# Optimization experiments

Hardware: AMD Instinct MI355X
Metric: run time of the kernel (lower is better)

The kernel has to match this reference:

```python
import jax, jax.numpy as jnp
import numpy as np

B, S, D = 4, 4096, 1024
E, H, TOPK = 8, 2752, 2


def setup_inputs() -> dict:
    key = jax.random.key(0)
    k0, k1, k2, k3, k4 = jax.random.split(key, 5)
    x = jax.random.normal(k0, (B, S, D), dtype=jnp.float32)
    gate_w = jax.random.normal(k1, (E, D), dtype=jnp.float32) * 0.02
    w1 = jax.random.normal(k2, (E, H, D), dtype=jnp.float32) * 0.02
    w2 = jax.random.normal(k3, (E, D, H), dtype=jnp.float32) * 0.02
    w3 = jax.random.normal(k4, (E, H, D), dtype=jnp.float32) * 0.02
    return {"x": x, "gate_w": gate_w, "w1": w1, "w2": w2, "w3": w3}


def reference(x, gate_w, w1, w2, w3):
    """MoE layer: softmax router -> top-k (normalized) -> per-expert SwiGLU FFN -> weighted combine."""
    b, s, d = x.shape
    xt = x.reshape(-1, d)                       # [T, D], T = B*S
    logits = xt @ gate_w.T                      # [T, E]
    scores = jax.nn.softmax(logits, axis=-1)
    topk_w, topk_i = jax.lax.top_k(scores, TOPK)  # [T, K]
    topk_w = topk_w / (jnp.sum(topk_w, axis=-1, keepdims=True) + 1e-20)

    y = jnp.zeros_like(xt)
    n_experts = gate_w.shape[0]
    for e in range(n_experts):
        # combine weight for expert e per token (0 if not routed to e)
        we = jnp.sum(jnp.where(topk_i == e, topk_w, 0.0), axis=-1)  # [T]
        h = jax.nn.silu(xt @ w1[e].T) * (xt @ w3[e].T)              # [T, H]
        y = y + we[:, None] * (h @ w2[e].T)                         # [T, D]
    return y.reshape(b, s, d)
```

## Files before the change

### kernel.cpp

```cpp
#include <hip/hip_runtime.h>
#include <hip/hip_bf16.h>
#include <stdint.h>

#define T_TOK 16384
#define D_DIM 1024
#define E_NUM 8
#define H_DIM 2752
#define NSLOT (T_TOK * 2)

typedef __bf16 bf16x8_t __attribute__((ext_vector_type(8)));
typedef float f32x4_t __attribute__((ext_vector_type(4)));

__device__ __forceinline__ uint16_t f2bf(float f) {
    union { float f; uint32_t u; } v; v.f = f;
    return (uint16_t)((v.u + 0x7FFFu + ((v.u >> 16) & 1u)) >> 16);
}
__device__ __forceinline__ ushort4 f4_to_bf4(float4 v) {
    ushort4 r; r.x = f2bf(v.x); r.y = f2bf(v.y); r.z = f2bf(v.z); r.w = f2bf(v.w);
    return r;
}
__device__ __forceinline__ void gl_lds16(const uint16_t* g, uint16_t* l) {
    __builtin_amdgcn_global_load_lds((const __attribute__((address_space(1))) void*)g,
                                     (__attribute__((address_space(3))) void*)l,
                                     16, 0, 0);
}

__global__ __launch_bounds__(256) void router_kernel(
    const float* __restrict__ x, const float* __restrict__ gw,
    int* __restrict__ topk_i, float* __restrict__ topk_w) {
    int tid = threadIdx.x;
    int t = blockIdx.x * 4 + (tid >> 6);
    int lane = tid & 63;
    const float* xr = x + (size_t)t * D_DIM;
    double acc[E_NUM];
#pragma unroll
    for (int e = 0; e < E_NUM; ++e) acc[e] = 0.0;
    for (int k = lane; k < D_DIM; k += 64) {
        double xv = (double)xr[k];
#pragma unroll
        for (int e = 0; e < E_NUM; ++e) acc[e] += xv * (double)gw[e * D_DIM + k];
    }
#pragma unroll
    for (int e = 0; e < E_NUM; ++e) {
        double v = acc[e];
        for (int off = 32; off > 0; off >>= 1) v += __shfl_down(v, off, 64);
        acc[e] = v;
    }
    if (lane == 0) {
        int i0 = 0; double m0 = acc[0];
#pragma unroll
        for (int e = 1; e < E_NUM; ++e) if (acc[e] > m0) { m0 = acc[e]; i0 = e; }
        int i1 = -1; double m1 = -1.0e300;
#pragma unroll
        for (int e = 0; e < E_NUM; ++e) if (e != i0 && acc[e] > m1) { m1 = acc[e]; i1 = e; }
        double e1 = exp(m1 - m0);
        double s = 1.0 + e1;
        topk_i[t * 2 + 0] = i0; topk_i[t * 2 + 1] = i1;
        topk_w[t * 2 + 0] = (float)(1.0 / s);
        topk_w[t * 2 + 1] = (float)(e1 / s);
    }
}

__global__ __launch_bounds__(256) void count_kernel(
    const int* __restrict__ topk_i,
    int* __restrict__ counts_f, int* __restrict__ counts_s) {
    __shared__ int hf[E_NUM], hs[E_NUM];
    int tid = threadIdx.x;
    if (tid < E_NUM) { hf[tid] = 0; hs[tid] = 0; }
    __syncthreads();
    int t = blockIdx.x * 256 + tid;
    atomicAdd(&hf[topk_i[t * 2 + 0]], 1);
    atomicAdd(&hs[topk_i[t * 2 + 1]], 1);
    __syncthreads();
    if (tid < E_NUM) {
        if (hf[tid]) atomicAdd(&counts_f[tid], hf[tid]);
    } else if (tid < 2 * E_NUM) {
        int e = tid - E_NUM;
        if (hs[e]) atomicAdd(&counts_s[e], hs[e]);
    }
}

__global__ void prefix_kernel(const int* __restrict__ cf, const int* __restrict__ cs,
                              int* __restrict__ bases, int* __restrict__ splits,
                              int* __restrict__ cnts) {
    int s = 0;
    for (int e = 0; e < E_NUM; ++e) {
        bases[e] = s;
        splits[e] = s + cf[e];
        cnts[e] = cf[e] + cs[e];
        s += cnts[e];
    }
}

__global__ __launch_bounds__(256) void assign_kernel(
    const int* __restrict__ topk_i, const float* __restrict__ topk_w,
    const int* __restrict__ bases, const int* __restrict__ splits,
    int* __restrict__ fills_f, int* __restrict__ fills_s,
    int* __restrict__ slot_tok, float* __restrict__ slot_w) {
    __shared__ int hf[E_NUM], hs[E_NUM], bf[E_NUM], bs[E_NUM];
    int tid = threadIdx.x;
    if (tid < E_NUM) { hf[tid] = 0; hs[tid] = 0; }
    __syncthreads();
    int t = blockIdx.x * 256 + tid;
    int e0 = topk_i[t * 2 + 0], e1 = topk_i[t * 2 + 1];
    int r0 = atomicAdd(&hf[e0], 1);
    int r1 = atomicAdd(&hs[e1], 1);
    __syncthreads();
    if (tid < E_NUM) {
        bf[tid] = hf[tid] ? atomicAdd(&fills_f[tid], hf[tid]) : 0;
    } else if (tid < 2 * E_NUM) {
        int e = tid - E_NUM;
        bs[e] = hs[e] ? atomicAdd(&fills_s[e], hs[e]) : 0;
    }
    __syncthreads();
    int s0 = bases[e0] + bf[e0] + r0;
    int s1 = splits[e1] + bs[e1] + r1;
    slot_tok[s0] = t; slot_w[s0] = topk_w[t * 2 + 0];
    slot_tok[s1] = t; slot_w[s1] = topk_w[t * 2 + 1];
}

__global__ __launch_bounds__(256) void cvtx_kernel(const float* __restrict__ x,
                                                   uint16_t* __restrict__ Xb) {
    size_t i = (size_t)blockIdx.x * 256 + threadIdx.x;
    ((ushort4*)Xb)[i] = f4_to_bf4(((const float4*)x)[i]);
}
__global__ __launch_bounds__(256) void cvt13_kernel(const float* __restrict__ w1,
                                                    const float* __restrict__ w3,
                                                    uint16_t* __restrict__ w1be,
                                                    uint16_t* __restrict__ w3be, int e) {
    size_t i = (size_t)blockIdx.x * 256 + threadIdx.x;
    const float4* s1 = (const float4*)(w1 + (size_t)e * H_DIM * D_DIM);
    const float4* s3 = (const float4*)(w3 + (size_t)e * H_DIM * D_DIM);
    ((ushort4*)w1be)[i] = f4_to_bf4(s1[i]);
    ((ushort4*)w3be)[i] = f4_to_bf4(s3[i]);
}
__global__ __launch_bounds__(256) void cvt2_kernel(const float* __restrict__ w2,
                                                   uint16_t* __restrict__ w2b) {
    size_t i = (size_t)blockIdx.x * 256 + threadIdx.x;
    ((ushort4*)w2b)[i] = f4_to_bf4(((const float4*)w2)[i]);
}

__global__ __launch_bounds__(256) void gemm1_kernel(
    const uint16_t* __restrict__ Xb, const uint16_t* __restrict__ w1be,
    const uint16_t* __restrict__ w3be, const int* __restrict__ slot_tok,
    const int* __restrict__ cnts, const int* __restrict__ bases,
    uint16_t* __restrict__ hidden, int e) {
    int cnt = cnts[e];
    int lin = blockIdx.y * 43 + blockIdx.x;
    int c = lin & 7, j = lin >> 3;
    int m_t = (j / 43) * 8 + c;
    int n_t = j % 43;
    int m0 = m_t * 128;
    if (m0 >= cnt) return;
    int n0 = n_t * 64;
    int base = bases[e];

    __shared__ __align__(16) uint16_t As[128 * 32];
    __shared__ __align__(16) uint16_t B1s[64 * 32];
    __shared__ __align__(16) uint16_t B3s[64 * 32];

    int tid = threadIdx.x;
    int w = tid >> 6, lane = tid & 63;
    int rA = lane & 15, kq = lane >> 4;
    int lr = lane >> 2, lc = lane & 3;

    int tok0 = slot_tok[base + min(m0 + w * 32 + lr, cnt - 1)];
    int tok1 = slot_tok[base + min(m0 + w * 32 + 16 + lr, cnt - 1)];
    const uint16_t* pA0 = Xb + (size_t)tok0 * D_DIM + lc * 8;
    const uint16_t* pA1 = Xb + (size_t)tok1 * D_DIM + lc * 8;
    const uint16_t* pB1 = w1be + (size_t)(n0 + w * 16 + lr) * D_DIM + lc * 8;
    const uint16_t* pB3 = w3be + (size_t)(n0 + w * 16 + lr) * D_DIM + lc * 8;
    uint16_t* lA0 = &As[(w * 2 + 0) * 512];
    uint16_t* lA1 = &As[(w * 2 + 1) * 512];
    uint16_t* lB1 = &B1s[w * 512];
    uint16_t* lB3 = &B3s[w * 512];

    f32x4_t acc1[2][4], acc3[2][4];
#pragma unroll
    for (int r = 0; r < 2; ++r)
#pragma unroll
        for (int n = 0; n < 4; ++n) {
            acc1[r][n] = (f32x4_t){0.f, 0.f, 0.f, 0.f};
            acc3[r][n] = (f32x4_t){0.f, 0.f, 0.f, 0.f};
        }

    for (int k0 = 0; k0 < D_DIM; k0 += 32) {
        __syncthreads();
        gl_lds16(pA0, lA0);
        gl_lds16(pA1, lA1);
        gl_lds16(pB1, lB1);
        gl_lds16(pB3, lB3);
        pA0 += 32; pA1 += 32; pB1 += 32; pB3 += 32;
        __syncthreads();

        bf16x8_t a0 = *(const bf16x8_t*)&As[(w * 32 + rA) * 32 + kq * 8];
        bf16x8_t a1 = *(const bf16x8_t*)&As[(w * 32 + 16 + rA) * 32 + kq * 8];
#pragma unroll
        for (int n = 0; n < 4; ++n) {
            bf16x8_t b1 = *(const bf16x8_t*)&B1s[(n * 16 + rA) * 32 + kq * 8];
            bf16x8_t b3 = *(const bf16x8_t*)&B3s[(n * 16 + rA) * 32 + kq * 8];
            acc1[0][n] = __builtin_amdgcn_mfma_f32_16x16x32_bf16(a0, b1, acc1[0][n], 0, 0, 0);
            acc1[1][n] = __builtin_amdgcn_mfma_f32_16x16x32_bf16(a1, b1, acc1[1][n], 0, 0, 0);
            acc3[0][n] = __builtin_amdgcn_mfma_f32_16x16x32_bf16(a0, b3, acc3[0][n], 0, 0, 0);
            acc3[1][n] = __builtin_amdgcn_mfma_f32_16x16x32_bf16(a1, b3, acc3[1][n], 0, 0, 0);
        }
    }

#pragma unroll
    for (int r = 0; r < 2; ++r)
#pragma unroll
        for (int n = 0; n < 4; ++n)
#pragma unroll
            for (int i = 0; i < 4; ++i) {
                int mrow = m0 + w * 32 + r * 16 + kq * 4 + i;
                if (mrow < cnt) {
                    float g = acc1[r][n][i];
                    float s = g / (1.0f + __expf(-g));
                    float h = s * acc3[r][n][i];
                    hidden[(size_t)(base + mrow) * H_DIM + n0 + n * 16 + rA] = f2bf(h);
                }
            }
}

__global__ __launch_bounds__(256) void gemm2_kernel(
    const uint16_t* __restrict__ hidden, const uint16_t* __restrict__ w2b,
    const int* __restrict__ cnts, const int* __restrict__ bases,
    const int* __restrict__ slot_tok, const float* __restrict__ slot_w,
    float* __restrict__ out) {
    int e = blockIdx.z;
    int cnt = cnts[e];
    int lin = blockIdx.y * 8 + blockIdx.x;
    int c = lin & 7, j = lin >> 3;
    int m_t = (j >> 3) * 8 + c;
    int x_t = j & 7;
    int m0 = m_t * 128;
    if (m0 >= cnt) return;
    int base = bases[e];
    int d0 = x_t * 128;

    __shared__ __align__(16) uint16_t As[128 * 32];
    __shared__ __align__(16) uint16_t Bs[128 * 32];

    int tid = threadIdx.x;
    int w = tid >> 6, lane = tid & 63;
    int rA = lane & 15, kq = lane >> 4;
    int lr = lane >> 2, lc = lane & 3;
    int mh = w & 1, nh = w >> 1;

    int sl0 = base + min(m0 + w * 32 + lr, cnt - 1);
    int sl1 = base + min(m0 + w * 32 + 16 + lr, cnt - 1);
    const uint16_t* pA0 = hidden + (size_t)sl0 * H_DIM + lc * 8;
    const uint16_t* pA1 = hidden + (size_t)sl1 * H_DIM + lc * 8;
    const uint16_t* pB0 = w2b + (size_t)(e * D_DIM + d0 + w * 32 + lr) * H_DIM + lc * 8;
    const uint16_t* pB1 = w2b + (size_t)(e * D_DIM + d0 + w * 32 + 16 + lr) * H_DIM + lc * 8;
    uint16_t* lA0 = &As[(w * 2 + 0) * 512];
    uint16_t* lA1 = &As[(w * 2 + 1) * 512];
    uint16_t* lB0 = &Bs[(w * 2 + 0) * 512];
    uint16_t* lB1 = &Bs[(w * 2 + 1) * 512];

    f32x4_t acc[4][4];
#pragma unroll
    for (int mf = 0; mf < 4; ++mf)
#pragma unroll
        for (int nf = 0; nf < 4; ++nf) acc[mf][nf] = (f32x4_t){0.f, 0.f, 0.f, 0.f};

    for (int k0 = 0; k0 < H_DIM; k0 += 32) {
        __syncthreads();
        gl_lds16(pA0, lA0);
        gl_lds16(pA1, lA1);
        gl_lds16(pB0, lB0);
        gl_lds16(pB1, lB1);
        pA0 += 32; pA1 += 32; pB0 += 32; pB1 += 32;
        __syncthreads();

        bf16x8_t a[4], b[4];
#pragma unroll
        for (int mf = 0; mf < 4; ++mf)
            a[mf] = *(const bf16x8_t*)&As[(mh * 64 + mf * 16 + rA) * 32 + kq * 8];
#pragma unroll
        for (int nf = 0; nf < 4; ++nf)
            b[nf] = *(const bf16x8_t*)&Bs[(nh * 64 + nf * 16 + rA) * 32 + kq * 8];
#pragma unroll
        for (int mf = 0; mf < 4; ++mf)
#pragma unroll
            for (int nf = 0; nf < 4; ++nf)
                acc[mf][nf] = __builtin_amdgcn_mfma_f32_16x16x32_bf16(a[mf], b[nf], acc[mf][nf], 0, 0, 0);
    }

#pragma unroll
    for (int mf = 0; mf < 4; ++mf)
#pragma unroll
        for (int i = 0; i < 4; ++i) {
            int mr = m0 + mh * 64 + mf * 16 + kq * 4 + i;
            if (mr < cnt) {
                int slot = base + mr;
                float wgt = slot_w[slot];
                int tok = slot_tok[slot];
                float* yr = out + (size_t)tok * D_DIM + d0 + nh * 64;
#pragma unroll
                for (int nf = 0; nf < 4; ++nf)
                    atomicAdd(&yr[nf * 16 + rA], wgt * acc[mf][nf][i]);
            }
        }
}

extern "C" void kernel_launch(void* const* d_in, const int* in_sizes, int n_in,
                              void* d_out, int out_size, void* d_ws, size_t ws_size,
                              hipStream_t stream) {
    const float* x  = (const float*)d_in[0];
    const float* gw = (const float*)d_in[1];
    const float* w1 = (const float*)d_in[2];
    const float* w2 = (const float*)d_in[3];
    const float* w3 = (const float*)d_in[4];
    float* out = (float*)d_out;
    char* ws = (char*)d_ws;

    int*   counts_f = (int*)(ws + 0);
    int*   counts_s = (int*)(ws + 256);
    int*   fills_f  = (int*)(ws + 512);
    int*   fills_s  = (int*)(ws + 768);
    int*   bases    = (int*)(ws + 1024);
    int*   splits   = (int*)(ws + 1280);
    int*   cnts     = (int*)(ws + 1536);
    int*   topk_i   = (int*)(ws + 4096);
    float* topk_w   = (float*)(ws + 4096 + 1 * 131072);
    int*   slot_tok = (int*)(ws + 4096 + 2 * 131072);
    float* slot_w   = (float*)(ws + 4096 + 3 * 131072);

    const size_t HID_OFF = 4ull << 20;
    const size_t W_OFF   = HID_OFF + (size_t)NSLOT * H_DIM * 2;
    const size_t W1SZ    = (size_t)H_DIM * D_DIM * 2;
    uint16_t* hidden = (uint16_t*)(ws + HID_OFF);
    uint16_t* w1be   = (uint16_t*)(ws + W_OFF);
    uint16_t* w3be   = (uint16_t*)(ws + W_OFF + W1SZ);
    uint16_t* Xb     = (uint16_t*)(ws + W_OFF + 2 * W1SZ);
    uint16_t* w2b    = (uint16_t*)(ws + W_OFF);

    hipMemsetAsync(ws, 0, 1024, stream);
    hipMemsetAsync(out, 0, (size_t)T_TOK * D_DIM * sizeof(float), stream);

    router_kernel<<<T_TOK / 4, 256, 0, stream>>>(x, gw, topk_i, topk_w);
    count_kernel<<<T_TOK / 256, 256, 0, stream>>>(topk_i, counts_f, counts_s);
    prefix_kernel<<<1, 1, 0, stream>>>(counts_f, counts_s, bases, splits, cnts);
    assign_kernel<<<T_TOK / 256, 256, 0, stream>>>(topk_i, topk_w, bases, splits,
                                                   fills_f, fills_s, slot_tok, slot_w);
    cvtx_kernel<<<T_TOK * D_DIM / 1024, 256, 0, stream>>>(x, Xb);

    for (int e = 0; e < E_NUM; ++e) {
        cvt13_kernel<<<H_DIM, 256, 0, stream>>>(w1, w3, w1be, w3be, e);
        gemm1_kernel<<<dim3(H_DIM / 64, 128), 256, 0, stream>>>(
            Xb, w1be, w3be, slot_tok, cnts, bases, hidden, e);
    }

    cvt2_kernel<<<E_NUM * D_DIM * H_DIM / 1024, 256, 0, stream>>>(w2, w2b);
    gemm2_kernel<<<dim3(8, 128, E_NUM), 256, 0, stream>>>(
        hidden, w2b, cnts, bases, slot_tok, slot_w, out);
}
```

Before: 1.358 ms.

## Batch gemm1 over groups of four experts and stage bf16 x in output buffer

Converts w1/w3 weights for four experts per launch and runs gemm1 with a z-dimension over those experts, cutting the per-expert launch sequence from eight pairs to two. Each launch then has more concurrent blocks, which reduces tail under-utilization when expert token counts are small. The bf16 copy of x now lives in the output buffer, so the workspace has room for four experts' weights, and the output memset moves after gemm1. The grid swizzle for L2 reuse is dropped in favour of plain block indexing.

```diff
diff --git a/kernel.cpp b/kernel.cpp
--- a/kernel.cpp
+++ b/kernel.cpp
@@ -124,15 +124,14 @@
     size_t i = (size_t)blockIdx.x * 256 + threadIdx.x;
     ((ushort4*)Xb)[i] = f4_to_bf4(((const float4*)x)[i]);
 }
-__global__ __launch_bounds__(256) void cvt13_kernel(const float* __restrict__ w1,
-                                                    const float* __restrict__ w3,
-                                                    uint16_t* __restrict__ w1be,
-                                                    uint16_t* __restrict__ w3be, int e) {
+__global__ __launch_bounds__(256) void cvt13g_kernel(const float* __restrict__ w1,
+                                                     const float* __restrict__ w3,
+                                                     uint16_t* __restrict__ w1be,
+                                                     uint16_t* __restrict__ w3be, int g) {
     size_t i = (size_t)blockIdx.x * 256 + threadIdx.x;
-    const float4* s1 = (const float4*)(w1 + (size_t)e * H_DIM * D_DIM);
-    const float4* s3 = (const float4*)(w3 + (size_t)e * H_DIM * D_DIM);
-    ((ushort4*)w1be)[i] = f4_to_bf4(s1[i]);
-    ((ushort4*)w3be)[i] = f4_to_bf4(s3[i]);
+    size_t off = (size_t)g * 4 * H_DIM * D_DIM / 4;
+    ((ushort4*)w1be)[i] = f4_to_bf4(((const float4*)w1)[off + i]);
+    ((ushort4*)w3be)[i] = f4_to_bf4(((const float4*)w3)[off + i]);
 }
 __global__ __launch_bounds__(256) void cvt2_kernel(const float* __restrict__ w2,
                                                    uint16_t* __restrict__ w2b) {
@@ -144,16 +143,16 @@
     const uint16_t* __restrict__ Xb, const uint16_t* __restrict__ w1be,
     const uint16_t* __restrict__ w3be, const int* __restrict__ slot_tok,
     const int* __restrict__ cnts, const int* __restrict__ bases,
-    uint16_t* __restrict__ hidden, int e) {
+    uint16_t* __restrict__ hidden, int g) {
+    int ez = blockIdx.z;
+    int e = g * 4 + ez;
     int cnt = cnts[e];
-    int lin = blockIdx.y * 43 + blockIdx.x;
-    int c = lin & 7, j = lin >> 3;
-    int m_t = (j / 43) * 8 + c;
-    int n_t = j % 43;
-    int m0 = m_t * 128;
+    int m0 = blockIdx.y * 128;
     if (m0 >= cnt) return;
-    int n0 = n_t * 64;
+    int n0 = blockIdx.x * 64;
     int base = bases[e];
+    const uint16_t* w1p = w1be + (size_t)ez * H_DIM * D_DIM;
+    const uint16_t* w3p = w3be + (size_t)ez * H_DIM * D_DIM;
 
     __shared__ __align__(16) uint16_t As[128 * 32];
     __shared__ __align__(16) uint16_t B1s[64 * 32];
@@ -168,8 +167,8 @@
     int tok1 = slot_tok[base + min(m0 + w * 32 + 16 + lr, cnt - 1)];
     const uint16_t* pA0 = Xb + (size_t)tok0 * D_DIM + lc * 8;
     const uint16_t* pA1 = Xb + (size_t)tok1 * D_DIM + lc * 8;
-    const uint16_t* pB1 = w1be + (size_t)(n0 + w * 16 + lr) * D_DIM + lc * 8;
-    const uint16_t* pB3 = w3be + (size_t)(n0 + w * 16 + lr) * D_DIM + lc * 8;
+    const uint16_t* pB1 = w1p + (size_t)(n0 + w * 16 + lr) * D_DIM + lc * 8;
+    const uint16_t* pB3 = w3p + (size_t)(n0 + w * 16 + lr) * D_DIM + lc * 8;
     uint16_t* lA0 = &As[(w * 2 + 0) * 512];
     uint16_t* lA1 = &As[(w * 2 + 1) * 512];
     uint16_t* lB1 = &B1s[w * 512];
@@ -214,8 +213,8 @@
             for (int i = 0; i < 4; ++i) {
                 int mrow = m0 + w * 32 + r * 16 + kq * 4 + i;
                 if (mrow < cnt) {
-                    float g = acc1[r][n][i];
-                    float s = g / (1.0f + __expf(-g));
+                    float gv = acc1[r][n][i];
+                    float s = gv / (1.0f + __expf(-gv));
                     float h = s * acc3[r][n][i];
                     hidden[(size_t)(base + mrow) * H_DIM + n0 + n * 16 + rA] = f2bf(h);
                 }
@@ -332,12 +331,11 @@
     const size_t W1SZ    = (size_t)H_DIM * D_DIM * 2;
     uint16_t* hidden = (uint16_t*)(ws + HID_OFF);
     uint16_t* w1be   = (uint16_t*)(ws + W_OFF);
-    uint16_t* w3be   = (uint16_t*)(ws + W_OFF + W1SZ);
-    uint16_t* Xb     = (uint16_t*)(ws + W_OFF + 2 * W1SZ);
+    uint16_t* w3be   = (uint16_t*)(ws + W_OFF + 4 * W1SZ);
     uint16_t* w2b    = (uint16_t*)(ws + W_OFF);
+    uint16_t* Xb     = (uint16_t*)d_out;
 
     hipMemsetAsync(ws, 0, 1024, stream);
-    hipMemsetAsync(out, 0, (size_t)T_TOK * D_DIM * sizeof(float), stream);
 
     router_kernel<<<T_TOK / 4, 256, 0, stream>>>(x, gw, topk_i, topk_w);
     count_kernel<<<T_TOK / 256, 256, 0, stream>>>(topk_i, counts_f, counts_s);
@@ -346,12 +344,13 @@
                                                    fills_f, fills_s, slot_tok, slot_w);
     cvtx_kernel<<<T_TOK * D_DIM / 1024, 256, 0, stream>>>(x, Xb);
 
-    for (int e = 0; e < E_NUM; ++e) {
-        cvt13_kernel<<<H_DIM, 256, 0, stream>>>(w1, w3, w1be, w3be, e);
-        gemm1_kernel<<<dim3(H_DIM / 64, 128), 256, 0, stream>>>(
-            Xb, w1be, w3be, slot_tok, cnts, bases, hidden, e);
-    }
-
+    for (int g = 0; g < 2; ++g) {
+        cvt13g_kernel<<<H_DIM * 4, 256, 0, stream>>>(w1, w3, w1be, w3be, g);
+        gemm1_kernel<<<dim3(H_DIM / 64, 128, 4), 256, 0, stream>>>(
+            Xb, w1be, w3be, slot_tok, cnts, bases, hidden, g);
+    }
+
+    hipMemsetAsync(out, 0, (size_t)T_TOK * D_DIM * sizeof(float), stream);
     cvt2_kernel<<<E_NUM * D_DIM * H_DIM / 1024, 256, 0, stream>>>(w2, w2b);
     gemm2_kernel<<<dim3(8, 128, E_NUM), 256, 0, stream>>>(
         hidden, w2b, cnts, bases, slot_tok, slot_w, out);
```

After: 1.240 ms. 8.7% less time.
